# Kernel tuning notes

Hardware: AMD Instinct MI355X
Metric: run time of the kernel (lower is better)

The kernel has to match this reference:

```python
import jax, jax.numpy as jnp
import numpy as np

L_MAX = 3
N_RADIAL = [2, 2, 1, 1]  # radial powers r^{2k} with 2k+l <= l_max=3


def fibonacci_sphere(n):
    i = np.arange(n, dtype=np.float64)
    phi = np.pi * (3.0 - np.sqrt(5.0))
    y = 1.0 - 2.0 * i / (n - 1)
    r = np.sqrt(np.maximum(1.0 - y * y, 0.0))
    th = phi * i
    pts = np.stack([np.cos(th) * r, y, np.sin(th) * r], -1)
    return jnp.asarray(pts, dtype=jnp.float32)


def real_sh(u):
    # real spherical harmonics on unit vectors u[...,3], degrees 0..3
    x, y, z = u[..., 0], u[..., 1], u[..., 2]
    Y0 = 0.28209479 * jnp.ones_like(x)[..., None]
    Y1 = 0.48860251 * jnp.stack([y, z, x], -1)
    Y2 = jnp.stack([
        1.09254843 * x * y,
        1.09254843 * y * z,
        0.31539157 * (3.0 * z * z - 1.0),
        1.09254843 * x * z,
        0.54627421 * (x * x - y * y)], -1)
    Y3 = jnp.stack([
        0.59004359 * y * (3.0 * x * x - y * y),
        2.89061144 * x * y * z,
        0.45704579 * y * (5.0 * z * z - 1.0),
        0.37317633 * z * (5.0 * z * z - 3.0),
        0.45704579 * x * (5.0 * z * z - 1.0),
        1.44530572 * z * (x * x - y * y),
        0.59004359 * x * (x * x - 3.0 * y * y)], -1)
    return [Y0, Y1, Y2, Y3]


def grid_sample_3d(vol, grid):
    # vol: [B, D, H, W]; grid: [B, d, h, w, 3], grid[...,0]->W, [...,1]->H, [...,2]->D
    # align_corners=True, zeros padding (torch.nn.functional.grid_sample semantics)
    B, Dv, Hv, Wv = vol.shape
    ix = (grid[..., 0] + 1.0) * 0.5 * (Wv - 1)
    iy = (grid[..., 1] + 1.0) * 0.5 * (Hv - 1)
    iz = (grid[..., 2] + 1.0) * 0.5 * (Dv - 1)
    x0f, y0f, z0f = jnp.floor(ix), jnp.floor(iy), jnp.floor(iz)
    wx, wy, wz = ix - x0f, iy - y0f, iz - z0f
    x0, y0, z0 = x0f.astype(jnp.int32), y0f.astype(jnp.int32), z0f.astype(jnp.int32)
    x1, y1, z1 = x0 + 1, y0 + 1, z0 + 1
    bidx = jnp.arange(B).reshape(B, 1, 1, 1)

    def tap(zi, yi, xi):
        m = ((zi >= 0) & (zi < Dv) & (yi >= 0) & (yi < Hv) & (xi >= 0) & (xi < Wv)).astype(vol.dtype)
        v = vol[bidx, jnp.clip(zi, 0, Dv - 1), jnp.clip(yi, 0, Hv - 1), jnp.clip(xi, 0, Wv - 1)]
        return v * m

    out = (tap(z0, y0, x0) * (1 - wz) * (1 - wy) * (1 - wx)
         + tap(z0, y0, x1) * (1 - wz) * (1 - wy) * wx
         + tap(z0, y1, x0) * (1 - wz) * wy * (1 - wx)
         + tap(z0, y1, x1) * (1 - wz) * wy * wx
         + tap(z1, y0, x0) * wz * (1 - wy) * (1 - wx)
         + tap(z1, y0, x1) * wz * (1 - wy) * wx
         + tap(z1, y1, x0) * wz * wy * (1 - wx)
         + tap(z1, y1, x1) * wz * wy * wx)
    return out


def setup_inputs() -> dict:
    key = jax.random.key(0)
    ks = jax.random.split(key, 12)
    B, H, W, D, S = 8, 32, 32, 32, 64
    x = jax.random.normal(ks[0], (B, H, W, D, 3), jnp.float32) * 0.35
    x_density = jax.random.uniform(ks[1], (B, H, W, D), jnp.float32)
    F = jax.random.normal(ks[2], (B, S, 256), jnp.float32) * 0.1
    def lin(k, i, o):
        return jax.random.normal(k, (i, o), jnp.float32) / np.sqrt(i)
    return {
        'x': x, 'x_density': x_density, 'F': F,
        'S2': fibonacci_sphere(S),
        'bw1': lin(ks[3], 256, 64), 'bb1': jnp.zeros((64,), jnp.float32),
        'bw2': lin(ks[4], 64, 3), 'bb2': jnp.zeros((3,), jnp.float32),
        'cw1': lin(ks[5], 256, 128), 'cb1': jnp.zeros((128,), jnp.float32),
        'cw2': lin(ks[6], 128, 64), 'cb2': jnp.zeros((64,), jnp.float32),
        'iw': lin(ks[7], 128, 3), 'ib': jnp.zeros((3,), jnp.float32),
    }


def reference(x, x_density, F, S2, bw1, bb1, bw2, bb2, cw1, cb1, cw2, cb2, iw, ib):
    B, H, W, D, _ = x.shape
    S = S2.shape[0]
    quad = (4.0 * jnp.pi) / S  # sphere quadrature weight for fibonacci samples
    Ybase = real_sh(S2)  # list of [S, 2l+1]

    # frame (E) branch: basis MLP -> type-1 SH coefficients -> normalize
    basis = jax.nn.relu(F @ bw1 + bb1) @ bw2 + bb2          # [B,S,3]
    E = jnp.einsum('vm,bvc->bmc', Ybase[1], basis) * quad   # [B,3,3]
    E = E / jnp.clip(jnp.linalg.norm(E, axis=-1, keepdims=True), 1e-6)

    # latent code branch: code MLP -> full SHT coefficients per degree l
    latent = jax.nn.relu(F @ cw1 + cb1) @ cw2 + cb2         # [B,S,64]
    coeffs = [jnp.einsum('vm,bvc->bmc', Ybase[l], latent) * quad for l in range(L_MAX + 1)]

    # zernike monomials of the grid points
    xf = x.reshape(B, -1, 3)                                # [B,V,3]
    r = jnp.linalg.norm(xf, axis=-1, keepdims=True)         # [B,V,1]
    u = xf / jnp.clip(r, 1e-6)
    Yx = real_sh(u)
    points_code = []
    points_inv = None
    for l in range(L_MAX + 1):
        Pl = Yx[l] * (r ** l)                               # solid harmonic [B,V,2l+1]
        rad = jnp.stack([r[..., 0] ** (2 * k) for k in range(N_RADIAL[l])], -1)  # [B,V,n_l]
        zl = Pl[..., :, None] * rad[..., None, :]           # [B,V,2l+1,n_l]
        p = jnp.einsum('bmi,bvmj->bvij', coeffs[l], zl)     # [B,V,64,n_l]
        p = p.reshape(B, p.shape[1], -1)
        points_code.append(p)
        if l == 1:
            points_inv = p                                  # [B,V,128]
    points_code = jnp.concatenate(points_code, -1)          # [B,V,384]

    pts = points_inv @ iw + ib                              # [B,V,3]
    coords = pts.reshape(B, H, W, D, 3)
    vol = x_density.reshape(B, H, W, D)
    sampled = grid_sample_3d(vol, coords)                   # [B,H,W,D]
    return sampled, E, coords, points_code
```

## Files before the change

### kernel.cpp

```cpp
#include <hip/hip_runtime.h>
#include <math.h>

#define OFF_E     262144
#define OFF_COORD 262216
#define OFF_CODE  1048648

#define QUAD 0.19634954084936207f

#define WS_H1 0
#define WS_H2 32768
#define WS_C  98304
#define WS_AB 106496

__global__ __launch_bounds__(256) void k_hidden(
    const float* __restrict__ F,
    const float* __restrict__ bw1, const float* __restrict__ bb1,
    const float* __restrict__ cw1, const float* __restrict__ cb1,
    float* __restrict__ ws)
{
    __shared__ float sF[8 * 256];
    const int blk = blockIdx.x;
    const int b   = blk >> 3;
    const int r0  = (blk & 7) * 8;
    const int tid = threadIdx.x;

    float* wsH1 = ws + WS_H1;
    float* wsH2 = ws + WS_H2;

    const float* Fb = F + ((size_t)b * 64 + r0) * 256;
    for (int i = tid; i < 2048; i += 256) sF[i] = Fb[i];
    __syncthreads();

    for (int e = tid; e < 512; e += 256) {
        const int v = e >> 6, k = e & 63;
        const float* fr = sF + v * 256;
        float acc = bb1[k];
        #pragma unroll 8
        for (int j = 0; j < 256; ++j) acc = fmaf(fr[j], bw1[j * 64 + k], acc);
        wsH1[((size_t)b * 64 + r0 + v) * 64 + k] = fmaxf(acc, 0.f);
    }
    for (int e = tid; e < 1024; e += 256) {
        const int v = e >> 7, k = e & 127;
        const float* fr = sF + v * 256;
        float acc = cb1[k];
        #pragma unroll 8
        for (int j = 0; j < 256; ++j) acc = fmaf(fr[j], cw1[j * 128 + k], acc);
        wsH2[((size_t)b * 64 + r0 + v) * 128 + k] = fmaxf(acc, 0.f);
    }
}

__global__ __launch_bounds__(512) void k_coeffs(
    const float* __restrict__ ws_in,
    const float* __restrict__ S2,
    const float* __restrict__ bw2, const float* __restrict__ bb2,
    const float* __restrict__ cw2, const float* __restrict__ cb2,
    const float* __restrict__ iw,
    float* __restrict__ ws_out, float* __restrict__ outE)
{
    __shared__ float sH2[64 * 128];
    __shared__ float sLat[64 * 64];
    __shared__ float sY[64 * 16];
    __shared__ float sBas[64 * 3];
    __shared__ float sC[16 * 64];
    __shared__ float sE[9];

    const int b = blockIdx.x, tid = threadIdx.x;
    const float* wsH1 = ws_in + WS_H1;
    const float* wsH2 = ws_in + WS_H2;
    float* wsC  = ws_out + WS_C;
    float* wsAB = ws_out + WS_AB;

    const float* H2b = wsH2 + (size_t)b * 8192;
    for (int i = tid; i < 8192; i += 512) sH2[i] = H2b[i];

    if (tid < 64) {
        const float x = S2[tid * 3 + 0], y = S2[tid * 3 + 1], z = S2[tid * 3 + 2];
        float* Yv = sY + tid * 16;
        Yv[0]  = 0.28209479f;
        Yv[1]  = 0.48860251f * y;
        Yv[2]  = 0.48860251f * z;
        Yv[3]  = 0.48860251f * x;
        Yv[4]  = 1.09254843f * x * y;
        Yv[5]  = 1.09254843f * y * z;
        Yv[6]  = 0.31539157f * (3.f * z * z - 1.f);
        Yv[7]  = 1.09254843f * x * z;
        Yv[8]  = 0.54627421f * (x * x - y * y);
        Yv[9]  = 0.59004359f * y * (3.f * x * x - y * y);
        Yv[10] = 2.89061144f * x * y * z;
        Yv[11] = 0.45704579f * y * (5.f * z * z - 1.f);
        Yv[12] = 0.37317633f * z * (5.f * z * z - 3.f);
        Yv[13] = 0.45704579f * x * (5.f * z * z - 1.f);
        Yv[14] = 1.44530572f * z * (x * x - y * y);
        Yv[15] = 0.59004359f * x * (x * x - 3.f * y * y);
    }

    float breg = 0.f;
    if (tid < 192) {
        const int v = tid / 3, c = tid % 3;
        const float* h1 = wsH1 + ((size_t)b * 64 + v) * 64;
        float acc = bb2[c];
        #pragma unroll 8
        for (int k = 0; k < 64; ++k) acc = fmaf(h1[k], bw2[k * 3 + c], acc);
        breg = acc;
    }
    __syncthreads();

    if (tid < 192) sBas[tid] = breg;

    for (int e = tid; e < 4096; e += 512) {
        const int v = e >> 6, i = e & 63;
        const float* h2 = sH2 + v * 128;
        float acc = cb2[i];
        #pragma unroll 8
        for (int k = 0; k < 128; ++k) acc = fmaf(h2[k], cw2[k * 64 + i], acc);
        sLat[e] = acc;
    }
    __syncthreads();

    for (int o = tid; o < 1024; o += 512) {
        const int m = o >> 6, i = o & 63;
        float acc = 0.f;
        #pragma unroll 8
        for (int v = 0; v < 64; ++v) acc = fmaf(sY[v * 16 + m], sLat[v * 64 + i], acc);
        acc *= QUAD;
        sC[o] = acc;
        wsC[(size_t)b * 1024 + o] = acc;
    }
    if (tid < 9) {
        const int m = tid / 3, c = tid % 3;
        float acc = 0.f;
        for (int v = 0; v < 64; ++v) acc = fmaf(sY[v * 16 + 1 + m], sBas[v * 3 + c], acc);
        sE[tid] = acc * QUAD;
    }
    __syncthreads();

    if (tid < 9) {
        const int m = tid / 3;
        const float e0 = sE[m * 3 + 0], e1 = sE[m * 3 + 1], e2 = sE[m * 3 + 2];
        const float n = sqrtf(e0 * e0 + e1 * e1 + e2 * e2);
        outE[b * 9 + tid] = sE[tid] / fmaxf(n, 1e-6f);
    }
    if (tid < 18) {
        const int which = tid / 9, mc = tid % 9;
        const int m = mc / 3, c = mc % 3;
        float acc = 0.f;
        #pragma unroll 8
        for (int i = 0; i < 64; ++i)
            acc = fmaf(sC[(1 + m) * 64 + i], iw[(2 * i + which) * 3 + c], acc);
        wsAB[b * 18 + tid] = acc;
    }
}

template <int NM, int MOFF, bool HASJ>
__device__ __forceinline__ void phaseC(const float* __restrict__ sC,
                                       const float* __restrict__ sZ,
                                       float* __restrict__ out,
                                       size_t base, int i, int j)
{
    float cr[NM];
    #pragma unroll
    for (int m = 0; m < NM; ++m) cr[m] = sC[(MOFF + m) * 64 + i];
    #pragma unroll 4
    for (int v = 0; v < 64; ++v) {
        const float* Z = sZ + v * 17;
        float acc = 0.f;
        #pragma unroll
        for (int m = 0; m < NM; ++m) acc = fmaf(cr[m], Z[MOFF + m], acc);
        if (HASJ && j) acc *= Z[16];
        out[base + (size_t)v * 384] = acc;
    }
}

__global__ __launch_bounds__(384) void k_points(
    const float* __restrict__ x, const float* __restrict__ dens,
    const float* __restrict__ ws, const float* __restrict__ ib,
    float* __restrict__ out)
{
    __shared__ float sC[16 * 64];
    __shared__ float sAB[18];
    __shared__ float sZ[64 * 17];

    const int blk = blockIdx.x;
    const int b   = blk >> 9;
    const int v0  = (blk & 511) * 64;
    const int tid = threadIdx.x;

    const float* wsC  = ws + WS_C;
    const float* wsAB = ws + WS_AB;

    for (int i = tid; i < 1024; i += 384) sC[i] = wsC[(size_t)b * 1024 + i];
    if (tid < 18) sAB[tid] = wsAB[b * 18 + tid];

    if (tid < 64) {
        const int v = v0 + tid;
        const size_t g = (size_t)b * 32768 + v;
        const float px = x[g * 3 + 0], py = x[g * 3 + 1], pz = x[g * 3 + 2];
        const float r2 = px * px + py * py + pz * pz;
        const float r  = sqrtf(r2);
        const float inv = 1.f / fmaxf(r, 1e-6f);
        const float ux = px * inv, uy = py * inv, uz = pz * inv;
        float* Z = sZ + tid * 17;
        Z[0] = 0.28209479f;
        Z[1] = 0.48860251f * uy * r;
        Z[2] = 0.48860251f * uz * r;
        Z[3] = 0.48860251f * ux * r;
        Z[4] = 1.09254843f * ux * uy * r2;
        Z[5] = 1.09254843f * uy * uz * r2;
        Z[6] = 0.31539157f * (3.f * uz * uz - 1.f) * r2;
        Z[7] = 1.09254843f * ux * uz * r2;
        Z[8] = 0.54627421f * (ux * ux - uy * uy) * r2;
        const float r3 = r2 * r;
        Z[9]  = 0.59004359f * uy * (3.f * ux * ux - uy * uy) * r3;
        Z[10] = 2.89061144f * ux * uy * uz * r3;
        Z[11] = 0.45704579f * uy * (5.f * uz * uz - 1.f) * r3;
        Z[12] = 0.37317633f * uz * (5.f * uz * uz - 3.f) * r3;
        Z[13] = 0.45704579f * ux * (5.f * uz * uz - 1.f) * r3;
        Z[14] = 1.44530572f * uz * (ux * ux - uy * uy) * r3;
        Z[15] = 0.59004359f * ux * (ux * ux - 3.f * uy * uy) * r3;
        Z[16] = r2;

        float pt[3];
        #pragma unroll
        for (int c = 0; c < 3; ++c) {
            float acc = ib[c];
            #pragma unroll
            for (int m = 0; m < 3; ++m)
                acc += Z[1 + m] * (sAB[m * 3 + c] + r2 * sAB[9 + m * 3 + c]);
            pt[c] = acc;
            out[OFF_COORD + g * 3 + c] = acc;
        }

        const float ix = (pt[0] + 1.f) * 0.5f * 31.f;
        const float iy = (pt[1] + 1.f) * 0.5f * 31.f;
        const float iz = (pt[2] + 1.f) * 0.5f * 31.f;
        const float x0f = floorf(ix), y0f = floorf(iy), z0f = floorf(iz);
        const float wx = ix - x0f, wy = iy - y0f, wz = iz - z0f;
        const int x0 = (int)x0f, y0 = (int)y0f, z0 = (int)z0f;
        const float* volb = dens + (size_t)b * 32768;
        float s = 0.f;
        #pragma unroll
        for (int dz = 0; dz < 2; ++dz) {
            const int zi = z0 + dz;
            const float wzz = dz ? wz : 1.f - wz;
            #pragma unroll
            for (int dy = 0; dy < 2; ++dy) {
                const int yi = y0 + dy;
                const float wyy = dy ? wy : 1.f - wy;
                #pragma unroll
                for (int dx = 0; dx < 2; ++dx) {
                    const int xi = x0 + dx;
                    const float wxx = dx ? wx : 1.f - wx;
                    if (zi >= 0 && zi < 32 && yi >= 0 && yi < 32 && xi >= 0 && xi < 32)
                        s += wzz * wyy * wxx * volb[zi * 1024 + yi * 32 + xi];
                }
            }
        }
        out[g] = s;
    }
    __syncthreads();

    const int c = tid;
    const size_t base = OFF_CODE + ((size_t)b * 32768 + v0) * 384 + c;
    if (c < 128) {
        phaseC<1, 0, true>(sC, sZ, out, base, c >> 1, c & 1);
    } else if (c < 256) {
        const int cc = c - 128;
        phaseC<3, 1, true>(sC, sZ, out, base, cc >> 1, cc & 1);
    } else if (c < 320) {
        phaseC<5, 4, false>(sC, sZ, out, base, c - 256, 0);
    } else {
        phaseC<7, 9, false>(sC, sZ, out, base, c - 320, 0);
    }
}

extern "C" void kernel_launch(void* const* d_in, const int* in_sizes, int n_in,
                              void* d_out, int out_size, void* d_ws, size_t ws_size,
                              hipStream_t stream) {
    const float* x    = (const float*)d_in[0];
    const float* dens = (const float*)d_in[1];
    const float* F    = (const float*)d_in[2];
    const float* S2   = (const float*)d_in[3];
    const float* bw1  = (const float*)d_in[4];
    const float* bb1  = (const float*)d_in[5];
    const float* bw2  = (const float*)d_in[6];
    const float* bb2  = (const float*)d_in[7];
    const float* cw1  = (const float*)d_in[8];
    const float* cb1  = (const float*)d_in[9];
    const float* cw2  = (const float*)d_in[10];
    const float* cb2  = (const float*)d_in[11];
    const float* iw   = (const float*)d_in[12];
    const float* ib   = (const float*)d_in[13];
    float* out = (float*)d_out;
    float* ws  = (float*)d_ws;

    k_hidden<<<64, 256, 0, stream>>>(F, bw1, bb1, cw1, cb1, ws);
    k_coeffs<<<8, 512, 0, stream>>>(ws, S2, bw2, bb2, cw2, cb2, iw, ws, out + OFF_E);
    k_points<<<4096, 384, 0, stream>>>(x, dens, ws, ib, out);
}
```

Before: 576.9 us.

## Vectorize MLP matvecs with float4 and enlarge point tiles with packed Z layout

k_hidden and k_coeffs now give each thread four output columns, reading weights as float4 and padding the shared rows to avoid bank conflicts. k_points handles 128 points per block instead of 64 and repacks the harmonic table into a 20-float stride so each band can be read with float4 loads. It also runs the coordinate and grid-sample work after the code-write loops so those loops are not held behind them, and folds the constant Y0 term into a scalar. The aim is fewer global weight loads and fewer LDS instructions, at the cost of more registers and fewer blocks in flight.

```diff
diff --git a/kernel.cpp b/kernel.cpp
--- a/kernel.cpp
+++ b/kernel.cpp
@@ -12,13 +12,13 @@
 #define WS_C  98304
 #define WS_AB 106496
 
-__global__ __launch_bounds__(256) void k_hidden(
+__global__ __launch_bounds__(384) void k_hidden(
     const float* __restrict__ F,
     const float* __restrict__ bw1, const float* __restrict__ bb1,
     const float* __restrict__ cw1, const float* __restrict__ cb1,
     float* __restrict__ ws)
 {
-    __shared__ float sF[8 * 256];
+    __shared__ float sF[8 * 257];
     const int blk = blockIdx.x;
     const int b   = blk >> 3;
     const int r0  = (blk & 7) * 8;
@@ -28,24 +28,42 @@
     float* wsH2 = ws + WS_H2;
 
     const float* Fb = F + ((size_t)b * 64 + r0) * 256;
-    for (int i = tid; i < 2048; i += 256) sF[i] = Fb[i];
-    __syncthreads();
-
-    for (int e = tid; e < 512; e += 256) {
-        const int v = e >> 6, k = e & 63;
-        const float* fr = sF + v * 256;
-        float acc = bb1[k];
-        #pragma unroll 8
-        for (int j = 0; j < 256; ++j) acc = fmaf(fr[j], bw1[j * 64 + k], acc);
-        wsH1[((size_t)b * 64 + r0 + v) * 64 + k] = fmaxf(acc, 0.f);
-    }
-    for (int e = tid; e < 1024; e += 256) {
-        const int v = e >> 7, k = e & 127;
-        const float* fr = sF + v * 256;
-        float acc = cb1[k];
-        #pragma unroll 8
-        for (int j = 0; j < 256; ++j) acc = fmaf(fr[j], cw1[j * 128 + k], acc);
-        wsH2[((size_t)b * 64 + r0 + v) * 128 + k] = fmaxf(acc, 0.f);
+    for (int i = tid; i < 2048; i += 384) sF[(i >> 8) * 257 + (i & 255)] = Fb[i];
+    __syncthreads();
+
+    if (tid < 128) {
+        const int row = tid >> 4, k4 = (tid & 15) * 4;
+        const float* fr = sF + row * 257;
+        float4 acc = *(const float4*)&bb1[k4];
+        #pragma unroll 4
+        for (int j = 0; j < 256; ++j) {
+            const float  f = fr[j];
+            const float4 w = *(const float4*)&bw1[j * 64 + k4];
+            acc.x = fmaf(f, w.x, acc.x);
+            acc.y = fmaf(f, w.y, acc.y);
+            acc.z = fmaf(f, w.z, acc.z);
+            acc.w = fmaf(f, w.w, acc.w);
+        }
+        acc.x = fmaxf(acc.x, 0.f); acc.y = fmaxf(acc.y, 0.f);
+        acc.z = fmaxf(acc.z, 0.f); acc.w = fmaxf(acc.w, 0.f);
+        *(float4*)&wsH1[((size_t)b * 64 + r0 + row) * 64 + k4] = acc;
+    } else {
+        const int tt  = tid - 128;
+        const int row = tt >> 5, k4 = (tt & 31) * 4;
+        const float* fr = sF + row * 257;
+        float4 acc = *(const float4*)&cb1[k4];
+        #pragma unroll 4
+        for (int j = 0; j < 256; ++j) {
+            const float  f = fr[j];
+            const float4 w = *(const float4*)&cw1[j * 128 + k4];
+            acc.x = fmaf(f, w.x, acc.x);
+            acc.y = fmaf(f, w.y, acc.y);
+            acc.z = fmaf(f, w.z, acc.z);
+            acc.w = fmaf(f, w.w, acc.w);
+        }
+        acc.x = fmaxf(acc.x, 0.f); acc.y = fmaxf(acc.y, 0.f);
+        acc.z = fmaxf(acc.z, 0.f); acc.w = fmaxf(acc.w, 0.f);
+        *(float4*)&wsH2[((size_t)b * 64 + r0 + row) * 128 + k4] = acc;
     }
 }
 
@@ -57,8 +75,8 @@
     const float* __restrict__ iw,
     float* __restrict__ ws_out, float* __restrict__ outE)
 {
-    __shared__ float sH2[64 * 128];
-    __shared__ float sLat[64 * 64];
+    __shared__ float sH2[64 * 129];
+    __shared__ alignas(16) float sLat[64 * 64];
     __shared__ float sY[64 * 16];
     __shared__ float sBas[64 * 3];
     __shared__ float sC[16 * 64];
@@ -71,7 +89,7 @@
     float* wsAB = ws_out + WS_AB;
 
     const float* H2b = wsH2 + (size_t)b * 8192;
-    for (int i = tid; i < 8192; i += 512) sH2[i] = H2b[i];
+    for (int i = tid; i < 8192; i += 512) sH2[(i >> 7) * 129 + (i & 127)] = H2b[i];
 
     if (tid < 64) {
         const float x = S2[tid * 3 + 0], y = S2[tid * 3 + 1], z = S2[tid * 3 + 2];
@@ -107,13 +125,20 @@
 
     if (tid < 192) sBas[tid] = breg;
 
-    for (int e = tid; e < 4096; e += 512) {
-        const int v = e >> 6, i = e & 63;
-        const float* h2 = sH2 + v * 128;
-        float acc = cb2[i];
-        #pragma unroll 8
-        for (int k = 0; k < 128; ++k) acc = fmaf(h2[k], cw2[k * 64 + i], acc);
-        sLat[e] = acc;
+    for (int t = tid; t < 1024; t += 512) {
+        const int row = t >> 4, i4 = (t & 15) * 4;
+        const float* h2 = sH2 + row * 129;
+        float4 acc = *(const float4*)&cb2[i4];
+        #pragma unroll 4
+        for (int k = 0; k < 128; ++k) {
+            const float  h = h2[k];
+            const float4 w = *(const float4*)&cw2[k * 64 + i4];
+            acc.x = fmaf(h, w.x, acc.x);
+            acc.y = fmaf(h, w.y, acc.y);
+            acc.z = fmaf(h, w.z, acc.z);
+            acc.w = fmaf(h, w.w, acc.w);
+        }
+        *(float4*)&sLat[row * 64 + i4] = acc;
     }
     __syncthreads();
 
@@ -151,83 +176,128 @@
     }
 }
 
-template <int NM, int MOFF, bool HASJ>
-__device__ __forceinline__ void phaseC(const float* __restrict__ sC,
-                                       const float* __restrict__ sZ,
-                                       float* __restrict__ out,
-                                       size_t base, int i, int j)
-{
-    float cr[NM];
-    #pragma unroll
-    for (int m = 0; m < NM; ++m) cr[m] = sC[(MOFF + m) * 64 + i];
-    #pragma unroll 4
-    for (int v = 0; v < 64; ++v) {
-        const float* Z = sZ + v * 17;
-        float acc = 0.f;
-        #pragma unroll
-        for (int m = 0; m < NM; ++m) acc = fmaf(cr[m], Z[MOFF + m], acc);
-        if (HASJ && j) acc *= Z[16];
-        out[base + (size_t)v * 384] = acc;
-    }
-}
-
 __global__ __launch_bounds__(384) void k_points(
     const float* __restrict__ x, const float* __restrict__ dens,
     const float* __restrict__ ws, const float* __restrict__ ib,
     float* __restrict__ out)
 {
-    __shared__ float sC[16 * 64];
+    __shared__ alignas(16) float sC[16 * 64];
     __shared__ float sAB[18];
-    __shared__ float sZ[64 * 17];
+    __shared__ alignas(16) float sZ[128 * 20];
 
     const int blk = blockIdx.x;
-    const int b   = blk >> 9;
-    const int v0  = (blk & 511) * 64;
+    const int b   = blk >> 8;
+    const int v0  = (blk & 255) * 128;
     const int tid = threadIdx.x;
 
     const float* wsC  = ws + WS_C;
     const float* wsAB = ws + WS_AB;
 
-    for (int i = tid; i < 1024; i += 384) sC[i] = wsC[(size_t)b * 1024 + i];
+    if (tid < 256) ((float4*)sC)[tid] = ((const float4*)(wsC + (size_t)b * 1024))[tid];
     if (tid < 18) sAB[tid] = wsAB[b * 18 + tid];
 
-    if (tid < 64) {
+    float z1 = 0.f, z2 = 0.f, z3 = 0.f, r2 = 0.f;
+    size_t g = 0;
+    if (tid < 128) {
         const int v = v0 + tid;
-        const size_t g = (size_t)b * 32768 + v;
+        g = (size_t)b * 32768 + v;
         const float px = x[g * 3 + 0], py = x[g * 3 + 1], pz = x[g * 3 + 2];
-        const float r2 = px * px + py * py + pz * pz;
-        const float r  = sqrtf(r2);
+        r2 = px * px + py * py + pz * pz;
+        const float r   = sqrtf(r2);
         const float inv = 1.f / fmaxf(r, 1e-6f);
         const float ux = px * inv, uy = py * inv, uz = pz * inv;
-        float* Z = sZ + tid * 17;
-        Z[0] = 0.28209479f;
-        Z[1] = 0.48860251f * uy * r;
-        Z[2] = 0.48860251f * uz * r;
-        Z[3] = 0.48860251f * ux * r;
-        Z[4] = 1.09254843f * ux * uy * r2;
-        Z[5] = 1.09254843f * uy * uz * r2;
-        Z[6] = 0.31539157f * (3.f * uz * uz - 1.f) * r2;
-        Z[7] = 1.09254843f * ux * uz * r2;
-        Z[8] = 0.54627421f * (ux * ux - uy * uy) * r2;
+        float* Z = sZ + tid * 20;
+        z1 = 0.48860251f * uy * r;
+        z2 = 0.48860251f * uz * r;
+        z3 = 0.48860251f * ux * r;
+        Z[0] = z1; Z[1] = z2; Z[2] = z3; Z[3] = r2;
         const float r3 = r2 * r;
-        Z[9]  = 0.59004359f * uy * (3.f * ux * ux - uy * uy) * r3;
-        Z[10] = 2.89061144f * ux * uy * uz * r3;
-        Z[11] = 0.45704579f * uy * (5.f * uz * uz - 1.f) * r3;
-        Z[12] = 0.37317633f * uz * (5.f * uz * uz - 3.f) * r3;
-        Z[13] = 0.45704579f * ux * (5.f * uz * uz - 1.f) * r3;
-        Z[14] = 1.44530572f * uz * (ux * ux - uy * uy) * r3;
-        Z[15] = 0.59004359f * ux * (ux * ux - 3.f * uy * uy) * r3;
-        Z[16] = r2;
-
+        Z[4]  = 0.59004359f * uy * (3.f * ux * ux - uy * uy) * r3;
+        Z[5]  = 2.89061144f * ux * uy * uz * r3;
+        Z[6]  = 0.45704579f * uy * (5.f * uz * uz - 1.f) * r3;
+        Z[7]  = 0.37317633f * uz * (5.f * uz * uz - 3.f) * r3;
+        Z[8]  = 0.45704579f * ux * (5.f * uz * uz - 1.f) * r3;
+        Z[9]  = 1.44530572f * uz * (ux * ux - uy * uy) * r3;
+        Z[10] = 0.59004359f * ux * (ux * ux - 3.f * uy * uy) * r3;
+        Z[12] = 1.09254843f * ux * uy * r2;
+        Z[13] = 1.09254843f * uy * uz * r2;
+        Z[14] = 0.31539157f * (3.f * uz * uz - 1.f) * r2;
+        Z[15] = 1.09254843f * ux * uz * r2;
+        Z[16] = 0.54627421f * (ux * ux - uy * uy) * r2;
+    }
+    __syncthreads();
+
+    const int c = tid;
+    float* po = out + OFF_CODE + ((size_t)b * 32768 + v0) * 384 + c;
+    if (c < 128) {
+        const float cr = sC[c >> 1] * 0.28209479f;
+        const bool  jr = (c & 1) != 0;
+        #pragma unroll 4
+        for (int v = 0; v < 128; ++v) {
+            const float r2v = sZ[v * 20 + 3];
+            const float a = jr ? cr * r2v : cr;
+            po[(size_t)v * 384] = a;
+        }
+    } else if (c < 256) {
+        const int  i  = (c - 128) >> 1;
+        const bool jr = (c & 1) != 0;
+        const float c0 = sC[1 * 64 + i], c1 = sC[2 * 64 + i], c2 = sC[3 * 64 + i];
+        #pragma unroll 4
+        for (int v = 0; v < 128; ++v) {
+            const float4 z = *(const float4*)(sZ + v * 20);
+            float a = c0 * z.x;
+            a = fmaf(c1, z.y, a);
+            a = fmaf(c2, z.z, a);
+            a = jr ? a * z.w : a;
+            po[(size_t)v * 384] = a;
+        }
+    } else if (c < 320) {
+        const int i = c - 256;
+        const float c0 = sC[4 * 64 + i], c1 = sC[5 * 64 + i], c2 = sC[6 * 64 + i];
+        const float c3 = sC[7 * 64 + i], c4 = sC[8 * 64 + i];
+        #pragma unroll 4
+        for (int v = 0; v < 128; ++v) {
+            const float4 z  = *(const float4*)(sZ + v * 20 + 12);
+            const float  z4 = sZ[v * 20 + 16];
+            float a = c0 * z.x;
+            a = fmaf(c1, z.y, a);
+            a = fmaf(c2, z.z, a);
+            a = fmaf(c3, z.w, a);
+            a = fmaf(c4, z4,  a);
+            po[(size_t)v * 384] = a;
+        }
+    } else {
+        const int i = c - 320;
+        const float c0 = sC[ 9 * 64 + i], c1 = sC[10 * 64 + i], c2 = sC[11 * 64 + i];
+        const float c3 = sC[12 * 64 + i], c4 = sC[13 * 64 + i], c5 = sC[14 * 64 + i];
+        const float c6 = sC[15 * 64 + i];
+        #pragma unroll 4
+        for (int v = 0; v < 128; ++v) {
+            const float4 za = *(const float4*)(sZ + v * 20 + 4);
+            const float2 zb = *(const float2*)(sZ + v * 20 + 8);
+            const float  zc = sZ[v * 20 + 10];
+            float a = c0 * za.x;
+            a = fmaf(c1, za.y, a);
+            a = fmaf(c2, za.z, a);
+            a = fmaf(c3, za.w, a);
+            a = fmaf(c4, zb.x, a);
+            a = fmaf(c5, zb.y, a);
+            a = fmaf(c6, zc,  a);
+            po[(size_t)v * 384] = a;
+        }
+    }
+
+    if (tid < 128) {
+        const float zr0 = z1, zr1 = z2, zr2 = z3;
         float pt[3];
         #pragma unroll
-        for (int c = 0; c < 3; ++c) {
-            float acc = ib[c];
-            #pragma unroll
-            for (int m = 0; m < 3; ++m)
-                acc += Z[1 + m] * (sAB[m * 3 + c] + r2 * sAB[9 + m * 3 + c]);
-            pt[c] = acc;
-            out[OFF_COORD + g * 3 + c] = acc;
+        for (int cc = 0; cc < 3; ++cc) {
+            float acc = ib[cc];
+            acc = fmaf(zr0, sAB[0 * 3 + cc] + r2 * sAB[9 + 0 * 3 + cc], acc);
+            acc = fmaf(zr1, sAB[1 * 3 + cc] + r2 * sAB[9 + 1 * 3 + cc], acc);
+            acc = fmaf(zr2, sAB[2 * 3 + cc] + r2 * sAB[9 + 2 * 3 + cc], acc);
+            pt[cc] = acc;
+            out[OFF_COORD + g * 3 + cc] = acc;
         }
 
         const float ix = (pt[0] + 1.f) * 0.5f * 31.f;
@@ -257,20 +327,6 @@
         }
         out[g] = s;
     }
-    __syncthreads();
-
-    const int c = tid;
-    const size_t base = OFF_CODE + ((size_t)b * 32768 + v0) * 384 + c;
-    if (c < 128) {
-        phaseC<1, 0, true>(sC, sZ, out, base, c >> 1, c & 1);
-    } else if (c < 256) {
-        const int cc = c - 128;
-        phaseC<3, 1, true>(sC, sZ, out, base, cc >> 1, cc & 1);
-    } else if (c < 320) {
-        phaseC<5, 4, false>(sC, sZ, out, base, c - 256, 0);
-    } else {
-        phaseC<7, 9, false>(sC, sZ, out, base, c - 320, 0);
-    }
 }
 
 extern "C" void kernel_launch(void* const* d_in, const int* in_sizes, int n_in,
@@ -293,7 +349,7 @@
     float* out = (float*)d_out;
     float* ws  = (float*)d_ws;
 
-    k_hidden<<<64, 256, 0, stream>>>(F, bw1, bb1, cw1, cb1, ws);
-    k_coeffs<<<8, 512, 0, stream>>>(ws, S2, bw2, bb2, cw2, cb2, iw, ws, out + OFF_E);
-    k_points<<<4096, 384, 0, stream>>>(x, dens, ws, ib, out);
+    k_hidden<<<64,   384, 0, stream>>>(F, bw1, bb1, cw1, cb1, ws);
+    k_coeffs<<<8,    512, 0, stream>>>(ws, S2, bw2, bb2, cw2, cb2, iw, ws, out + OFF_E);
+    k_points<<<2048, 384, 0, stream>>>(x, dens, ws, ib, out);
 }
```

Result: no change. 588.0 us (+1.9%).
